# Performance work log

Measured on AMD Instinct MI355X. Metric: run time of the kernel, lower is better.

Reference implementation:

```python
import jax, jax.numpy as jnp
import numpy as np

B, N, C = 16, 4096, 512
PW, PH = 64, 64  # N = PW * PH
POOL = 2         # attention_pool_scale
D_SCALE = 1.0 / float(np.sqrt(C))


def setup_inputs() -> dict:
    key = jax.random.key(0)
    ks = jax.random.split(key, 4)
    w_std = 1.0 / float(np.sqrt(C))
    return {
        "x": jax.random.normal(ks[0], (B, N, C), dtype=jnp.float32),
        "Wq": jax.random.normal(ks[1], (C, C), dtype=jnp.float32) * w_std,
        "bq": jnp.zeros((C,), dtype=jnp.float32),
        "Wk": jax.random.normal(ks[2], (C, C), dtype=jnp.float32) * w_std,
        "bk": jnp.zeros((C,), dtype=jnp.float32),
        "Wv": jax.random.normal(ks[3], (C, C), dtype=jnp.float32) * w_std,
        "bv": jnp.zeros((C,), dtype=jnp.float32),
    }


def _to_spatial(t):
    # [B, N, C] -> [B, C, PW, PH]
    return t.transpose(0, 2, 1).reshape(t.shape[0], C, PW, PH)


def reference(x, Wq, bq, Wk, bk, Wv, bv):
    # Linear (torch convention y = x @ W^T + b) + sigmoid activation
    def proj(W, b):
        return jax.nn.sigmoid(jnp.einsum('bnc,dc->bnd', x, W) + b)

    Q = _to_spatial(proj(Wq, bq))  # [B, C, PW, PH]
    K = _to_spatial(proj(Wk, bk))
    V = _to_spatial(proj(Wv, bv))

    # avg_pool2d with kernel (POOL, 1): pool over PW axis
    q = Q.reshape(B, C, PW // POOL, POOL, PH).mean(axis=3)  # [B, C, PW/2, PH]
    k = K.reshape(B, C, PW // POOL, POOL, PH).mean(axis=3)

    # Qk = softmax(scale * Q @ k^T): [B, C, PW, PW/2]
    Qk = jax.nn.softmax(D_SCALE * jnp.einsum('bcik,bcjk->bcij', Q, k), axis=-1)
    # Kq = softmax(scale * q @ K^T): [B, C, PW/2, PW]
    Kq = jax.nn.softmax(D_SCALE * jnp.einsum('bcik,bcjk->bcij', q, K), axis=-1)
    # Kqv = Kq @ V: [B, C, PW/2, PH]
    Kqv = jnp.einsum('bcij,bcjk->bcik', Kq, V)
    # out = Qk @ Kqv: [B, C, PW, PH]
    out = jnp.einsum('bcij,bcjk->bcik', Qk, Kqv)

    # spatial -> sequence: [B, C, PW*PH] -> [B, N, C]
    return out.reshape(B, C, N).transpose(0, 2, 1)
```

## Files before the change

kernel.cpp:

```cpp
#include <hip/hip_runtime.h>
#include <hip/hip_bf16.h>
#include <string.h>

typedef __hip_bfloat16  bf16;
typedef __hip_bfloat162 bf162;
typedef __attribute__((ext_vector_type(8))) short short8;
typedef __attribute__((ext_vector_type(4))) float f32x4;

#define NB 16
#define NN 4096
#define NC 512
#define SCALE 0.044194173824159216f

#define GLL16(gp, lp) __builtin_amdgcn_global_load_lds( \
    (__attribute__((address_space(1))) void*)(gp),      \
    (__attribute__((address_space(3))) void*)(lp), 16, 0, 0)

__global__ __launch_bounds__(256) void cast_x_kernel(
    const float* __restrict__ x, bf16* __restrict__ xb)
{
    size_t i = ((size_t)blockIdx.x * 256 + threadIdx.x) * 8;
    float4 a = *(const float4*)(x + i);
    float4 b = *(const float4*)(x + i + 4);
    bf16 t[8];
    t[0] = __float2bfloat16(a.x); t[1] = __float2bfloat16(a.y);
    t[2] = __float2bfloat16(a.z); t[3] = __float2bfloat16(a.w);
    t[4] = __float2bfloat16(b.x); t[5] = __float2bfloat16(b.y);
    t[6] = __float2bfloat16(b.z); t[7] = __float2bfloat16(b.w);
    uint4 r; memcpy(&r, t, 16);
    *(uint4*)(xb + i) = r;
}

__global__ __launch_bounds__(256) void cast_w_kernel(
    const float* __restrict__ Wq, const float* __restrict__ Wk,
    const float* __restrict__ Wv, bf16* __restrict__ Wb)
{
    const float* W = (blockIdx.y == 0) ? Wq : (blockIdx.y == 1) ? Wk : Wv;
    size_t i = ((size_t)blockIdx.x * 256 + threadIdx.x) * 8;
    float4 a = *(const float4*)(W + i);
    float4 b = *(const float4*)(W + i + 4);
    bf16 t[8];
    t[0] = __float2bfloat16(a.x); t[1] = __float2bfloat16(a.y);
    t[2] = __float2bfloat16(a.z); t[3] = __float2bfloat16(a.w);
    t[4] = __float2bfloat16(b.x); t[5] = __float2bfloat16(b.y);
    t[6] = __float2bfloat16(b.z); t[7] = __float2bfloat16(b.w);
    uint4 r; memcpy(&r, t, 16);
    *(uint4*)(Wb + (size_t)blockIdx.y * (NC * NC) + i) = r;
}

__global__ __launch_bounds__(256) void proj_mfma(
    const bf16* __restrict__ xb, const bf16* __restrict__ Wb,
    const float* __restrict__ bq, const float* __restrict__ bk,
    const float* __restrict__ bv,
    bf16* __restrict__ Qs, bf16* __restrict__ Ks, bf16* __restrict__ Vs)
{
    __shared__ __align__(16) char smem[36864];
    short* As = (short*)smem;
    short* Bs = (short*)(smem + 16384);
    bf16*  OutS = (bf16*)smem;

    const int tid = threadIdx.x;
    const int w   = tid >> 6;
    const int l   = tid & 63;
    const int q   = l >> 4;
    const int mrow= l & 15;
    const int wr  = w >> 1;
    const int wc  = w & 1;

    const int bx = blockIdx.x;
    const int m  = bx >> 2;
    const int d0 = (bx & 3) * 128;
    const int r0 = blockIdx.y * 128;
    const int b  = r0 >> 12;
    const int n0 = r0 & 4095;

    const bf16*  W    = Wb + (size_t)m * (NC * NC);
    const float* bias = (m == 0) ? bq : (m == 1) ? bk : bv;
    bf16*        Out  = (m == 0) ? Qs : (m == 1) ? Ks : Vs;

    f32x4 acc[4][4];
    const f32x4 z = {0.f, 0.f, 0.f, 0.f};
    #pragma unroll
    for (int i = 0; i < 4; ++i)
        #pragma unroll
        for (int j = 0; j < 4; ++j) acc[i][j] = z;

    const int srow = tid >> 3;
    const int scol = (tid & 7) * 8;
    const int sxor = ((tid ^ (tid >> 3)) & 7) * 8;
    const int axor = (mrow & 7) * 8;

    for (int k0 = 0; k0 < NC; k0 += 64) {
        #pragma unroll
        for (int c = 0; c < 4; ++c) {
            int row = srow + 32 * c;
            GLL16(xb + (size_t)(r0 + row) * NC + k0 + sxor, &As[row * 64 + scol]);
        }
        #pragma unroll
        for (int c = 0; c < 4; ++c) {
            int row = srow + 32 * c;
            GLL16(W + (size_t)(d0 + row) * NC + k0 + sxor, &Bs[row * 64 + scol]);
        }
        __syncthreads();

        #pragma unroll
        for (int ks = 0; ks < 2; ++ks) {
            short8 af[4], bfr[4];
            #pragma unroll
            for (int ti = 0; ti < 4; ++ti)
                af[ti] = *(const short8*)&As[(64 * wr + 16 * ti + mrow) * 64 +
                                             ((q * 8 + 32 * ks) ^ axor)];
            #pragma unroll
            for (int tj = 0; tj < 4; ++tj)
                bfr[tj] = *(const short8*)&Bs[(64 * wc + 16 * tj + mrow) * 64 +
                                              ((q * 8 + 32 * ks) ^ axor)];
            #pragma unroll
            for (int ti = 0; ti < 4; ++ti)
                #pragma unroll
                for (int tj = 0; tj < 4; ++tj)
                    acc[ti][tj] = __builtin_amdgcn_mfma_f32_16x16x32_bf16(
                        af[ti], bfr[tj], acc[ti][tj], 0, 0, 0);
        }
        __syncthreads();
    }

    float bb[4];
    #pragma unroll
    for (int tj = 0; tj < 4; ++tj) bb[tj] = bias[d0 + 64 * wc + 16 * tj + mrow];

    #pragma unroll
    for (int ti = 0; ti < 4; ++ti)
        #pragma unroll
        for (int tj = 0; tj < 4; ++tj) {
            int d = 64 * wc + 16 * tj + mrow;
            bf16 t4[4];
            #pragma unroll
            for (int g = 0; g < 4; ++g) {
                float v = acc[ti][tj][g] + bb[tj];
                t4[g] = __float2bfloat16(1.0f / (1.0f + __expf(-v)));
            }
            uint2 pk; memcpy(&pk, t4, 8);
            *(uint2*)&OutS[d * 144 + 64 * wr + 16 * ti + 4 * q] = pk;
        }
    __syncthreads();

    #pragma unroll
    for (int v = 0; v < 8; ++v) {
        int e  = tid + 256 * v;
        int d  = e >> 4;
        int ch = e & 15;
        uint4 r = *(const uint4*)&OutS[d * 144 + ch * 8];
        *(uint4*)(Out + ((size_t)b * NC + d0 + d) * NN + n0 + ch * 8) = r;
    }
}

__global__ __launch_bounds__(256) void attn_mfma(
    const bf16* __restrict__ Qs, const bf16* __restrict__ Ks,
    const bf16* __restrict__ Vs, bf16* __restrict__ Os)
{
    __shared__ __align__(16) char smem[24064];
    bf16* VT  = (bf16*)smem;
    bf16* S1b = (bf16*)(smem + 9216);
    bf16* S2b = (bf16*)(smem + 9216 + 5120);
    bf16* KVT = (bf16*)(smem + 9216 + 5120 + 4608);

    const int tid = threadIdx.x;
    const int w   = tid >> 6;
    const int l   = tid & 63;
    const int m   = l & 15;
    const int q   = l >> 4;
    const size_t base = (size_t)blockIdx.x * NN;

    {
        const uint4* src = (const uint4*)(Vs + base);
        #pragma unroll
        for (int v = 0; v < 2; ++v) {
            int e = tid + 256 * v;
            uint4 r = src[e];
            bf16 tmp[8]; memcpy(tmp, &r, 16);
            int pw = e >> 3;
            int a  = e & 7;
            int cs = (((pw >> 3) ^ a) & 7) << 3;
            int c7 = pw & 7;
            #pragma unroll
            for (int t = 0; t < 8; ++t)
                VT[(8 * a + t) * 72 + cs + c7] = tmp[t];
        }
    }

    f32x4 tacc[4];
    {
        const f32x4 z = {0.f, 0.f, 0.f, 0.f};
        short8 aQ[2];
        #pragma unroll
        for (int ks = 0; ks < 2; ++ks)
            aQ[ks] = *(const short8*)(Qs + base + (16 * w + m) * 64 + q * 8 + 32 * ks);
        __builtin_amdgcn_s_setprio(1);
        #pragma unroll
        for (int tj = 0; tj < 4; ++tj) {
            tacc[tj] = z;
            #pragma unroll
            for (int ks = 0; ks < 2; ++ks) {
                short8 bK = *(const short8*)(Ks + base + (16 * tj + m) * 64 + q * 8 + 32 * ks);
                tacc[tj] = __builtin_amdgcn_mfma_f32_16x16x32_bf16(aQ[ks], bK, tacc[tj], 0, 0, 0);
            }
        }
        __builtin_amdgcn_s_setprio(0);
    }

    {
        float p[4][4], e[4][4], mx[4], s[4];
        #pragma unroll
        for (int r = 0; r < 4; ++r) mx[r] = -1e30f;
        #pragma unroll
        for (int t = 0; t < 4; ++t)
            #pragma unroll
            for (int r = 0; r < 4; ++r) {
                float v  = tacc[t][r];
                float pv = (v + __shfl_xor(v, 1)) * (0.5f * SCALE);
                p[t][r] = pv;
                mx[r]   = fmaxf(mx[r], pv);
            }
        #pragma unroll
        for (int r = 0; r < 4; ++r) {
            #pragma unroll
            for (int d = 1; d < 16; d <<= 1)
                mx[r] = fmaxf(mx[r], __shfl_xor(mx[r], d));
            s[r] = 0.f;
        }
        #pragma unroll
        for (int t = 0; t < 4; ++t)
            #pragma unroll
            for (int r = 0; r < 4; ++r) {
                e[t][r] = __expf(p[t][r] - mx[r]);
                s[r] += e[t][r];
            }
        #pragma unroll
        for (int r = 0; r < 4; ++r) {
            #pragma unroll
            for (int d = 1; d < 16; d <<= 1)
                s[r] += __shfl_xor(s[r], d);
            s[r] = 2.0f / s[r];
        }
        if (!(l & 1)) {
            int jc = m >> 1;
            #pragma unroll
            for (int t = 0; t < 4; ++t)
                #pragma unroll
                for (int r = 0; r < 4; ++r)
                    S1b[(16 * w + q * 4 + r) * 40 + t * 8 + jc] =
                        __float2bfloat16(e[t][r] * s[r]);
        }
    }

    {
        float p2[4][2], e2[4][2], mx[2], s[2];
        #pragma unroll
        for (int h = 0; h < 2; ++h) mx[h] = -1e30f;
        #pragma unroll
        for (int t = 0; t < 4; ++t)
            #pragma unroll
            for (int h = 0; h < 2; ++h) {
                float pv = (tacc[t][2 * h] + tacc[t][2 * h + 1]) * (0.5f * SCALE);
                p2[t][h] = pv;
                mx[h]    = fmaxf(mx[h], pv);
            }
        #pragma unroll
        for (int h = 0; h < 2; ++h) {
            #pragma unroll
            for (int d = 1; d < 16; d <<= 1)
                mx[h] = fmaxf(mx[h], __shfl_xor(mx[h], d));
            s[h] = 0.f;
        }
        #pragma unroll
        for (int t = 0; t < 4; ++t)
            #pragma unroll
            for (int h = 0; h < 2; ++h) {
                e2[t][h] = __expf(p2[t][h] - mx[h]);
                s[h] += e2[t][h];
            }
        #pragma unroll
        for (int h = 0; h < 2; ++h) {
            #pragma unroll
            for (int d = 1; d < 16; d <<= 1)
                s[h] += __shfl_xor(s[h], d);
            s[h] = 1.0f / s[h];
        }
        #pragma unroll
        for (int t = 0; t < 4; ++t)
            #pragma unroll
            for (int h = 0; h < 2; ++h)
                S2b[(8 * w + q * 2 + h) * 72 + t * 16 + m] =
                    __float2bfloat16(e2[t][h] * s[h]);
    }
    __syncthreads();

    {
        const int rb = (2 * w + (m >> 3)) & 7;
        short8 aV[2];
        #pragma unroll
        for (int ks = 0; ks < 2; ++ks)
            aV[ks] = *(const short8*)&VT[(16 * w + m) * 72 +
                                         (((q + 4 * ks) ^ rb) & 7) * 8];
        __builtin_amdgcn_s_setprio(1);
        #pragma unroll
        for (int tn = 0; tn < 2; ++tn) {
            f32x4 kacc = {0.f, 0.f, 0.f, 0.f};
            #pragma unroll
            for (int ks = 0; ks < 2; ++ks) {
                short8 bS = *(const short8*)&S2b[(16 * tn + m) * 72 + q * 8 + 32 * ks];
                kacc = __builtin_amdgcn_mfma_f32_16x16x32_bf16(aV[ks], bS, kacc, 0, 0, 0);
            }
            #pragma unroll
            for (int r = 0; r < 4; ++r)
                KVT[(16 * w + q * 4 + r) * 40 + 16 * tn + m] = __float2bfloat16(kacc[r]);
        }
        __builtin_amdgcn_s_setprio(0);
    }
    __syncthreads();

    f32x4 oacc[4];
    {
        short8 aS = *(const short8*)&S1b[(16 * w + m) * 40 + q * 8];
        __builtin_amdgcn_s_setprio(1);
        #pragma unroll
        for (int tn = 0; tn < 4; ++tn) {
            short8 bKV = *(const short8*)&KVT[(16 * tn + m) * 40 + q * 8];
            f32x4 z = {0.f, 0.f, 0.f, 0.f};
            oacc[tn] = __builtin_amdgcn_mfma_f32_16x16x32_bf16(aS, bKV, z, 0, 0, 0);
        }
        __builtin_amdgcn_s_setprio(0);
    }

    {
        bf16* OutS = VT;
        #pragma unroll
        for (int tn = 0; tn < 4; ++tn)
            #pragma unroll
            for (int r = 0; r < 4; ++r)
                OutS[(16 * w + q * 4 + r) * 72 + 16 * tn + m] = __float2bfloat16(oacc[tn][r]);
        __syncthreads();
        uint* Og = (uint*)(Os + base);
        #pragma unroll
        for (int v = 0; v < 8; ++v) {
            int e  = tid + 256 * v;
            int i  = e >> 5;
            int pp = e & 31;
            Og[e] = *(uint*)&OutS[i * 72 + 2 * pp];
        }
    }
}

__global__ __launch_bounds__(256) void unspat_kernel(
    const bf16* __restrict__ Os, float* __restrict__ out)
{
    __shared__ float t[32][65];
    const int b  = blockIdx.z;
    const int c0 = blockIdx.y * 32;
    const int n0 = blockIdx.x * 64;
    const int tx = threadIdx.x & 31;
    const int ty = threadIdx.x >> 5;
    const bf162* src = (const bf162*)(Os + ((size_t)b * NC + c0) * NN + n0);
    #pragma unroll
    for (int r = 0; r < 4; ++r) {
        int cc = ty + r * 8;
        float2 f = __bfloat1622float2(src[(size_t)cc * (NN/2) + tx]);
        t[cc][2*tx] = f.x; t[cc][2*tx+1] = f.y;
    }
    __syncthreads();
    float* dst = out + ((size_t)b * NN + n0) * NC + c0;
    #pragma unroll
    for (int r = 0; r < 8; ++r) {
        int nn = ty + r * 8;
        dst[(size_t)nn * NC + tx] = t[tx][nn];
    }
}

extern "C" void kernel_launch(void* const* d_in, const int* in_sizes, int n_in,
                              void* d_out, int out_size, void* d_ws, size_t ws_size,
                              hipStream_t stream)
{
    const float* x  = (const float*)d_in[0];
    const float* Wq = (const float*)d_in[1];
    const float* bq = (const float*)d_in[2];
    const float* Wk = (const float*)d_in[3];
    const float* bk = (const float*)d_in[4];
    const float* Wv = (const float*)d_in[5];
    const float* bv = (const float*)d_in[6];
    float* out = (float*)d_out;

    const size_t S = (size_t)NB * NC * NN;
    bf16* Qb = (bf16*)d_ws;
    bf16* Kb = Qb + S;
    bf16* Vb = Kb + S;
    bf16* xb = (bf16*)d_out;
    bf16* Wb = ((bf16*)d_out) + S;

    cast_x_kernel<<<dim3((NB * NN * NC) / (256 * 8)), 256, 0, stream>>>(x, xb);
    cast_w_kernel<<<dim3((NC * NC) / (256 * 8), 3), 256, 0, stream>>>(Wq, Wk, Wv, Wb);
    proj_mfma<<<dim3(12, (NB * NN) / 128), 256, 0, stream>>>(
        xb, Wb, bq, bk, bv, Qb, Kb, Vb);
    attn_mfma<<<dim3(NB * NC), 256, 0, stream>>>(Qb, Kb, Vb, Qb);
    unspat_kernel<<<dim3(NN / 64, NC / 32, NB), 256, 0, stream>>>(Qb, out);
}
```

Before: 495.3 us.

## Process eight channels per attention block with register prefetch of next channel

```diff
diff --git a/kernel.cpp b/kernel.cpp
--- a/kernel.cpp
+++ b/kernel.cpp
@@ -10,6 +10,7 @@
 #define NB 16
 #define NN 4096
 #define NC 512
+#define NCH 8
 #define SCALE 0.044194173824159216f
 
 #define GLL16(gp, lp) __builtin_amdgcn_global_load_lds( \
@@ -169,184 +170,216 @@
     const int l   = tid & 63;
     const int m   = l & 15;
     const int q   = l >> 4;
-    const size_t base = (size_t)blockIdx.x * NN;
-
+    const size_t base0 = (size_t)blockIdx.x * NCH * NN;
+
+    uint4  vpre[2];
+    short8 qpre[2];
+    short8 kpre[8];
     {
-        const uint4* src = (const uint4*)(Vs + base);
-        #pragma unroll
-        for (int v = 0; v < 2; ++v) {
-            int e = tid + 256 * v;
-            uint4 r = src[e];
-            bf16 tmp[8]; memcpy(tmp, &r, 16);
-            int pw = e >> 3;
-            int a  = e & 7;
-            int cs = (((pw >> 3) ^ a) & 7) << 3;
-            int c7 = pw & 7;
-            #pragma unroll
-            for (int t = 0; t < 8; ++t)
-                VT[(8 * a + t) * 72 + cs + c7] = tmp[t];
-        }
-    }
-
-    f32x4 tacc[4];
-    {
-        const f32x4 z = {0.f, 0.f, 0.f, 0.f};
-        short8 aQ[2];
+        const uint4* src = (const uint4*)(Vs + base0);
+        vpre[0] = src[tid];
+        vpre[1] = src[tid + 256];
         #pragma unroll
         for (int ks = 0; ks < 2; ++ks)
-            aQ[ks] = *(const short8*)(Qs + base + (16 * w + m) * 64 + q * 8 + 32 * ks);
-        __builtin_amdgcn_s_setprio(1);
-        #pragma unroll
-        for (int tj = 0; tj < 4; ++tj) {
-            tacc[tj] = z;
-            #pragma unroll
-            for (int ks = 0; ks < 2; ++ks) {
-                short8 bK = *(const short8*)(Ks + base + (16 * tj + m) * 64 + q * 8 + 32 * ks);
-                tacc[tj] = __builtin_amdgcn_mfma_f32_16x16x32_bf16(aQ[ks], bK, tacc[tj], 0, 0, 0);
-            }
-        }
-        __builtin_amdgcn_s_setprio(0);
-    }
-
-    {
-        float p[4][4], e[4][4], mx[4], s[4];
-        #pragma unroll
-        for (int r = 0; r < 4; ++r) mx[r] = -1e30f;
-        #pragma unroll
-        for (int t = 0; t < 4; ++t)
+            qpre[ks] = *(const short8*)(Qs + base0 + (16 * w + m) * 64 + q * 8 + 32 * ks);
+        #pragma unroll
+        for (int tj = 0; tj < 4; ++tj)
+            #pragma unroll
+            for (int ks = 0; ks < 2; ++ks)
+                kpre[tj * 2 + ks] = *(const short8*)(Ks + base0 + (16 * tj + m) * 64 + q * 8 + 32 * ks);
+    }
+
+    for (int ch = 0; ch < NCH; ++ch) {
+        const size_t base = base0 + (size_t)ch * NN;
+        if (ch) __syncthreads();
+
+        {
+            #pragma unroll
+            for (int v = 0; v < 2; ++v) {
+                int e = tid + 256 * v;
+                bf16 tmp[8]; memcpy(tmp, &vpre[v], 16);
+                int pw = e >> 3;
+                int a  = e & 7;
+                int cs = (((pw >> 3) ^ a) & 7) << 3;
+                int c7 = pw & 7;
+                #pragma unroll
+                for (int t = 0; t < 8; ++t)
+                    VT[(8 * a + t) * 72 + cs + c7] = tmp[t];
+            }
+        }
+        if (ch + 1 < NCH) {
+            const uint4* srcn = (const uint4*)(Vs + base + NN);
+            vpre[0] = srcn[tid];
+            vpre[1] = srcn[tid + 256];
+        }
+
+        f32x4 tacc[4];
+        {
+            const f32x4 z = {0.f, 0.f, 0.f, 0.f};
+            __builtin_amdgcn_s_setprio(1);
+            #pragma unroll
+            for (int tj = 0; tj < 4; ++tj) {
+                tacc[tj] = z;
+                #pragma unroll
+                for (int ks = 0; ks < 2; ++ks)
+                    tacc[tj] = __builtin_amdgcn_mfma_f32_16x16x32_bf16(
+                        qpre[ks], kpre[tj * 2 + ks], tacc[tj], 0, 0, 0);
+            }
+            __builtin_amdgcn_s_setprio(0);
+        }
+        if (ch + 1 < NCH) {
+            const bf16* Qn = Qs + base + NN;
+            const bf16* Kn = Ks + base + NN;
+            #pragma unroll
+            for (int ks = 0; ks < 2; ++ks)
+                qpre[ks] = *(const short8*)(Qn + (16 * w + m) * 64 + q * 8 + 32 * ks);
+            #pragma unroll
+            for (int tj = 0; tj < 4; ++tj)
+                #pragma unroll
+                for (int ks = 0; ks < 2; ++ks)
+                    kpre[tj * 2 + ks] = *(const short8*)(Kn + (16 * tj + m) * 64 + q * 8 + 32 * ks);
+        }
+
+        {
+            float p[4][4], e[4][4], mx[4], s[4];
+            #pragma unroll
+            for (int r = 0; r < 4; ++r) mx[r] = -1e30f;
+            #pragma unroll
+            for (int t = 0; t < 4; ++t)
+                #pragma unroll
+                for (int r = 0; r < 4; ++r) {
+                    float v  = tacc[t][r];
+                    float pv = (v + __shfl_xor(v, 1)) * (0.5f * SCALE);
+                    p[t][r] = pv;
+                    mx[r]   = fmaxf(mx[r], pv);
+                }
             #pragma unroll
             for (int r = 0; r < 4; ++r) {
-                float v  = tacc[t][r];
-                float pv = (v + __shfl_xor(v, 1)) * (0.5f * SCALE);
-                p[t][r] = pv;
-                mx[r]   = fmaxf(mx[r], pv);
-            }
-        #pragma unroll
-        for (int r = 0; r < 4; ++r) {
-            #pragma unroll
-            for (int d = 1; d < 16; d <<= 1)
-                mx[r] = fmaxf(mx[r], __shfl_xor(mx[r], d));
-            s[r] = 0.f;
-        }
-        #pragma unroll
-        for (int t = 0; t < 4; ++t)
+                #pragma unroll
+                for (int d = 1; d < 16; d <<= 1)
+                    mx[r] = fmaxf(mx[r], __shfl_xor(mx[r], d));
+                s[r] = 0.f;
+            }
+            #pragma unroll
+            for (int t = 0; t < 4; ++t)
+                #pragma unroll
+                for (int r = 0; r < 4; ++r) {
+                    e[t][r] = __expf(p[t][r] - mx[r]);
+                    s[r] += e[t][r];
+                }
             #pragma unroll
             for (int r = 0; r < 4; ++r) {
-                e[t][r] = __expf(p[t][r] - mx[r]);
-                s[r] += e[t][r];
-            }
-        #pragma unroll
-        for (int r = 0; r < 4; ++r) {
-            #pragma unroll
-            for (int d = 1; d < 16; d <<= 1)
-                s[r] += __shfl_xor(s[r], d);
-            s[r] = 2.0f / s[r];
-        }
-        if (!(l & 1)) {
-            int jc = m >> 1;
+                #pragma unroll
+                for (int d = 1; d < 16; d <<= 1)
+                    s[r] += __shfl_xor(s[r], d);
+                s[r] = 2.0f / s[r];
+            }
+            if (!(l & 1)) {
+                int jc = m >> 1;
+                #pragma unroll
+                for (int t = 0; t < 4; ++t)
+                    #pragma unroll
+                    for (int r = 0; r < 4; ++r)
+                        S1b[(16 * w + q * 4 + r) * 40 + t * 8 + jc] =
+                            __float2bfloat16(e[t][r] * s[r]);
+            }
+        }
+
+        {
+            float p2[4][2], e2[4][2], mx[2], s[2];
+            #pragma unroll
+            for (int h = 0; h < 2; ++h) mx[h] = -1e30f;
             #pragma unroll
             for (int t = 0; t < 4; ++t)
                 #pragma unroll
+                for (int h = 0; h < 2; ++h) {
+                    float pv = (tacc[t][2 * h] + tacc[t][2 * h + 1]) * (0.5f * SCALE);
+                    p2[t][h] = pv;
+                    mx[h]    = fmaxf(mx[h], pv);
+                }
+            #pragma unroll
+            for (int h = 0; h < 2; ++h) {
+                #pragma unroll
+                for (int d = 1; d < 16; d <<= 1)
+                    mx[h] = fmaxf(mx[h], __shfl_xor(mx[h], d));
+                s[h] = 0.f;
+            }
+            #pragma unroll
+            for (int t = 0; t < 4; ++t)
+                #pragma unroll
+                for (int h = 0; h < 2; ++h) {
+                    e2[t][h] = __expf(p2[t][h] - mx[h]);
+                    s[h] += e2[t][h];
+                }
+            #pragma unroll
+            for (int h = 0; h < 2; ++h) {
+                #pragma unroll
+                for (int d = 1; d < 16; d <<= 1)
+                    s[h] += __shfl_xor(s[h], d);
+                s[h] = 1.0f / s[h];
+            }
+            #pragma unroll
+            for (int t = 0; t < 4; ++t)
+                #pragma unroll
+                for (int h = 0; h < 2; ++h)
+                    S2b[(8 * w + q * 2 + h) * 72 + t * 16 + m] =
+                        __float2bfloat16(e2[t][h] * s[h]);
+        }
+        __syncthreads();
+
+        {
+            const int rb = (2 * w + (m >> 3)) & 7;
+            short8 aV[2];
+            #pragma unroll
+            for (int ks = 0; ks < 2; ++ks)
+                aV[ks] = *(const short8*)&VT[(16 * w + m) * 72 +
+                                             (((q + 4 * ks) ^ rb) & 7) * 8];
+            __builtin_amdgcn_s_setprio(1);
+            #pragma unroll
+            for (int tn = 0; tn < 2; ++tn) {
+                f32x4 kacc = {0.f, 0.f, 0.f, 0.f};
+                #pragma unroll
+                for (int ks = 0; ks < 2; ++ks) {
+                    short8 bS = *(const short8*)&S2b[(16 * tn + m) * 72 + q * 8 + 32 * ks];
+                    kacc = __builtin_amdgcn_mfma_f32_16x16x32_bf16(aV[ks], bS, kacc, 0, 0, 0);
+                }
+                #pragma unroll
                 for (int r = 0; r < 4; ++r)
-                    S1b[(16 * w + q * 4 + r) * 40 + t * 8 + jc] =
-                        __float2bfloat16(e[t][r] * s[r]);
-        }
-    }
-
-    {
-        float p2[4][2], e2[4][2], mx[2], s[2];
-        #pragma unroll
-        for (int h = 0; h < 2; ++h) mx[h] = -1e30f;
-        #pragma unroll
-        for (int t = 0; t < 4; ++t)
-            #pragma unroll
-            for (int h = 0; h < 2; ++h) {
-                float pv = (tacc[t][2 * h] + tacc[t][2 * h + 1]) * (0.5f * SCALE);
-                p2[t][h] = pv;
-                mx[h]    = fmaxf(mx[h], pv);
-            }
-        #pragma unroll
-        for (int h = 0; h < 2; ++h) {
-            #pragma unroll
-            for (int d = 1; d < 16; d <<= 1)
-                mx[h] = fmaxf(mx[h], __shfl_xor(mx[h], d));
-            s[h] = 0.f;
-        }
-        #pragma unroll
-        for (int t = 0; t < 4; ++t)
-            #pragma unroll
-            for (int h = 0; h < 2; ++h) {
-                e2[t][h] = __expf(p2[t][h] - mx[h]);
-                s[h] += e2[t][h];
-            }
-        #pragma unroll
-        for (int h = 0; h < 2; ++h) {
-            #pragma unroll
-            for (int d = 1; d < 16; d <<= 1)
-                s[h] += __shfl_xor(s[h], d);
-            s[h] = 1.0f / s[h];
-        }
-        #pragma unroll
-        for (int t = 0; t < 4; ++t)
-            #pragma unroll
-            for (int h = 0; h < 2; ++h)
-                S2b[(8 * w + q * 2 + h) * 72 + t * 16 + m] =
-                    __float2bfloat16(e2[t][h] * s[h]);
-    }
-    __syncthreads();
-
-    {
-        const int rb = (2 * w + (m >> 3)) & 7;
-        short8 aV[2];
-        #pragma unroll
-        for (int ks = 0; ks < 2; ++ks)
-            aV[ks] = *(const short8*)&VT[(16 * w + m) * 72 +
-                                         (((q + 4 * ks) ^ rb) & 7) * 8];
-        __builtin_amdgcn_s_setprio(1);
-        #pragma unroll
-        for (int tn = 0; tn < 2; ++tn) {
-            f32x4 kacc = {0.f, 0.f, 0.f, 0.f};
-            #pragma unroll
-            for (int ks = 0; ks < 2; ++ks) {
-                short8 bS = *(const short8*)&S2b[(16 * tn + m) * 72 + q * 8 + 32 * ks];
-                kacc = __builtin_amdgcn_mfma_f32_16x16x32_bf16(aV[ks], bS, kacc, 0, 0, 0);
-            }
-            #pragma unroll
-            for (int r = 0; r < 4; ++r)
-                KVT[(16 * w + q * 4 + r) * 40 + 16 * tn + m] = __float2bfloat16(kacc[r]);
-        }
-        __builtin_amdgcn_s_setprio(0);
-    }
-    __syncthreads();
-
-    f32x4 oacc[4];
-    {
-        short8 aS = *(const short8*)&S1b[(16 * w + m) * 40 + q * 8];
-        __builtin_amdgcn_s_setprio(1);
-        #pragma unroll
-        for (int tn = 0; tn < 4; ++tn) {
-            short8 bKV = *(const short8*)&KVT[(16 * tn + m) * 40 + q * 8];
-            f32x4 z = {0.f, 0.f, 0.f, 0.f};
-            oacc[tn] = __builtin_amdgcn_mfma_f32_16x16x32_bf16(aS, bKV, z, 0, 0, 0);
-        }
-        __builtin_amdgcn_s_setprio(0);
-    }
-
-    {
-        bf16* OutS = VT;
-        #pragma unroll
-        for (int tn = 0; tn < 4; ++tn)
-            #pragma unroll
-            for (int r = 0; r < 4; ++r)
-                OutS[(16 * w + q * 4 + r) * 72 + 16 * tn + m] = __float2bfloat16(oacc[tn][r]);
+                    KVT[(16 * w + q * 4 + r) * 40 + 16 * tn + m] = __float2bfloat16(kacc[r]);
+            }
+            __builtin_amdgcn_s_setprio(0);
+        }
         __syncthreads();
-        uint* Og = (uint*)(Os + base);
-        #pragma unroll
-        for (int v = 0; v < 8; ++v) {
-            int e  = tid + 256 * v;
-            int i  = e >> 5;
-            int pp = e & 31;
-            Og[e] = *(uint*)&OutS[i * 72 + 2 * pp];
+
+        f32x4 oacc[4];
+        {
+            short8 aS = *(const short8*)&S1b[(16 * w + m) * 40 + q * 8];
+            __builtin_amdgcn_s_setprio(1);
+            #pragma unroll
+            for (int tn = 0; tn < 4; ++tn) {
+                short8 bKV = *(const short8*)&KVT[(16 * tn + m) * 40 + q * 8];
+                f32x4 z = {0.f, 0.f, 0.f, 0.f};
+                oacc[tn] = __builtin_amdgcn_mfma_f32_16x16x32_bf16(aS, bKV, z, 0, 0, 0);
+            }
+            __builtin_amdgcn_s_setprio(0);
+        }
+
+        {
+            bf16* OutS = VT;
+            #pragma unroll
+            for (int tn = 0; tn < 4; ++tn)
+                #pragma unroll
+                for (int r = 0; r < 4; ++r)
+                    OutS[(16 * w + q * 4 + r) * 72 + 16 * tn + m] = __float2bfloat16(oacc[tn][r]);
+            __syncthreads();
+            uint* Og = (uint*)(Os + base);
+            #pragma unroll
+            for (int v = 0; v < 8; ++v) {
+                int e  = tid + 256 * v;
+                int i  = e >> 5;
+                int pp = e & 31;
+                Og[e] = *(uint*)&OutS[i * 72 + 2 * pp];
+            }
         }
     }
 }
@@ -400,6 +433,6 @@
     cast_w_kernel<<<dim3((NC * NC) / (256 * 8), 3), 256, 0, stream>>>(Wq, Wk, Wv, Wb);
     proj_mfma<<<dim3(12, (NB * NN) / 128), 256, 0, stream>>>(
         xb, Wb, bq, bk, bv, Qb, Kb, Vb);
-    attn_mfma<<<dim3(NB * NC), 256, 0, stream>>>(Qb, Kb, Vb, Qb);
+    attn_mfma<<<dim3((NB * NC) / NCH), 256, 0, stream>>>(Qb, Kb, Vb, Qb);
     unspat_kernel<<<dim3(NN / 64, NC / 32, NB), 256, 0, stream>>>(Qb, out);
 }
```

After: 509.0 us. 1.03x slower.

## Store attention output transposed directly to global and fix up in unspatialize

Applied to the files above, without the earlier changes.

```diff
diff --git a/kernel.cpp b/kernel.cpp
--- a/kernel.cpp
+++ b/kernel.cpp
@@ -309,17 +309,18 @@
             #pragma unroll
             for (int ks = 0; ks < 2; ++ks) {
                 short8 bS = *(const short8*)&S2b[(16 * tn + m) * 72 + q * 8 + 32 * ks];
-                kacc = __builtin_amdgcn_mfma_f32_16x16x32_bf16(aV[ks], bS, kacc, 0, 0, 0);
-            }
-            #pragma unroll
-            for (int r = 0; r < 4; ++r)
-                KVT[(16 * w + q * 4 + r) * 40 + 16 * tn + m] = __float2bfloat16(kacc[r]);
+                kacc = __builtin_amdgcn_mfma_f32_16x16x32_bf16(bS, aV[ks], kacc, 0, 0, 0);
+            }
+            bf16 t4[4];
+            #pragma unroll
+            for (int r = 0; r < 4; ++r) t4[r] = __float2bfloat16(kacc[r]);
+            uint2 pk; memcpy(&pk, t4, 8);
+            *(uint2*)&KVT[(16 * w + m) * 40 + 16 * tn + 4 * q] = pk;
         }
         __builtin_amdgcn_s_setprio(0);
     }
     __syncthreads();
 
-    f32x4 oacc[4];
     {
         short8 aS = *(const short8*)&S1b[(16 * w + m) * 40 + q * 8];
         __builtin_amdgcn_s_setprio(1);
@@ -327,27 +328,14 @@
         for (int tn = 0; tn < 4; ++tn) {
             short8 bKV = *(const short8*)&KVT[(16 * tn + m) * 40 + q * 8];
             f32x4 z = {0.f, 0.f, 0.f, 0.f};
-            oacc[tn] = __builtin_amdgcn_mfma_f32_16x16x32_bf16(aS, bKV, z, 0, 0, 0);
+            f32x4 oacc = __builtin_amdgcn_mfma_f32_16x16x32_bf16(aS, bKV, z, 0, 0, 0);
+            bf16 t4[4];
+            #pragma unroll
+            for (int r = 0; r < 4; ++r) t4[r] = __float2bfloat16(oacc[r]);
+            uint2 pk; memcpy(&pk, t4, 8);
+            *(uint2*)(Os + base + (size_t)(16 * tn + m) * 64 + 16 * w + 4 * q) = pk;
         }
         __builtin_amdgcn_s_setprio(0);
-    }
-
-    {
-        bf16* OutS = VT;
-        #pragma unroll
-        for (int tn = 0; tn < 4; ++tn)
-            #pragma unroll
-            for (int r = 0; r < 4; ++r)
-                OutS[(16 * w + q * 4 + r) * 72 + 16 * tn + m] = __float2bfloat16(oacc[tn][r]);
-        __syncthreads();
-        uint* Og = (uint*)(Os + base);
-        #pragma unroll
-        for (int v = 0; v < 8; ++v) {
-            int e  = tid + 256 * v;
-            int i  = e >> 5;
-            int pp = e & 31;
-            Og[e] = *(uint*)&OutS[i * 72 + 2 * pp];
-        }
     }
 }
 
@@ -357,10 +345,11 @@
     __shared__ float t[32][65];
     const int b  = blockIdx.z;
     const int c0 = blockIdx.y * 32;
-    const int n0 = blockIdx.x * 64;
+    const int bx = blockIdx.x;
+    const int a0 = bx * 64;
     const int tx = threadIdx.x & 31;
     const int ty = threadIdx.x >> 5;
-    const bf162* src = (const bf162*)(Os + ((size_t)b * NC + c0) * NN + n0);
+    const bf162* src = (const bf162*)(Os + ((size_t)b * NC + c0) * NN + a0);
     #pragma unroll
     for (int r = 0; r < 4; ++r) {
         int cc = ty + r * 8;
@@ -368,11 +357,11 @@
         t[cc][2*tx] = f.x; t[cc][2*tx+1] = f.y;
     }
     __syncthreads();
-    float* dst = out + ((size_t)b * NN + n0) * NC + c0;
+    float* dstB = out + ((size_t)b * NN) * NC + c0;
     #pragma unroll
     for (int r = 0; r < 8; ++r) {
         int nn = ty + r * 8;
-        dst[(size_t)nn * NC + tx] = t[tx][nn];
+        dstB[(size_t)(nn * 64 + bx) * NC + tx] = t[tx][nn];
     }
 }
 
```

Result: no change. 500.5 us (+1.0%).
